# Optimization experiments

Hardware: AMD Instinct MI355X
Metric: run time of the kernel (lower is better)

The kernel has to match this reference:

```python
import jax, jax.numpy as jnp
import numpy as np

N, E, D = 50000, 800000, 64


def setup_inputs() -> dict:
    key = jax.random.key(0)
    ks = jax.random.split(key, 24)
    s = 1.0 / np.sqrt(D)
    inp = {
        'x': jax.random.normal(ks[0], (N, D), dtype=jnp.float32),
        'edge_index': jax.random.randint(ks[1], (2, E), 0, N, dtype=jnp.int32),
        'edge_attr_emb': jax.random.normal(ks[2], (E, D), dtype=jnp.float32),
    }
    names = ['Wq1', 'Wk1', 'Wv1', 'We1', 'Ws1', 'Wq2', 'Wk2', 'Wv2', 'We2', 'Ws2']
    for i, n in enumerate(names):
        inp[n] = jax.random.normal(ks[3 + i], (D, D), dtype=jnp.float32) * s
    for n in ['bq1', 'bk1', 'bv1', 'bs1', 'bq2', 'bk2', 'bv2', 'bs2']:
        inp[n] = jnp.zeros((D,), dtype=jnp.float32)
    return inp


def transformer_conv(x, src, dst, ea, Wq, bq, Wk, bk, Wv, bv, We, Ws, bs):
    # PyG TransformerConv, heads=1, concat=True, beta=False, root_weight=True
    q = x @ Wq + bq                      # [N, D]
    k = x @ Wk + bk                      # [N, D]
    v = x @ Wv + bv                      # [N, D]
    e = ea @ We                          # [E, D] (lin_edge has no bias)
    k_e = k[src] + e                     # gather source keys, modulate by edge
    logits = jnp.sum(q[dst] * k_e, axis=-1) / jnp.sqrt(jnp.asarray(D, x.dtype))  # [E]
    m = jax.ops.segment_max(logits, dst, num_segments=N)   # per-target max
    a = jnp.exp(logits - m[dst])
    denom = jax.ops.segment_sum(a, dst, num_segments=N)
    alpha = a / denom[dst]               # segment softmax over incoming edges
    msg = (v[src] + e) * alpha[:, None]  # [E, D]
    out = jax.ops.segment_sum(msg, dst, num_segments=N)    # scatter-add
    return out + x @ Ws + bs             # root/skip connection


def reference(x, edge_index, edge_attr_emb,
              Wq1, bq1, Wk1, bk1, Wv1, bv1, We1, Ws1, bs1,
              Wq2, bq2, Wk2, bk2, Wv2, bv2, We2, Ws2, bs2):
    src, dst = edge_index[0], edge_index[1]
    r = jax.nn.relu(x)
    r = transformer_conv(r, src, dst, edge_attr_emb, Wq1, bq1, Wk1, bk1, Wv1, bv1, We1, Ws1, bs1)
    r = jax.nn.relu(r)
    r = transformer_conv(r, src, dst, edge_attr_emb, Wq2, bq2, Wk2, bk2, Wv2, bv2, We2, Ws2, bs2)
    return x + r  # identity residual since l_in == l_out
```

## Files before the change

kernel.cpp:

```cpp
#include <hip/hip_runtime.h>
#include <math.h>

#define NN 50000
#define EE 800000
#define SCAN_B 196

__global__ __launch_bounds__(256) void k_hist(const int* __restrict__ ei,
                                              int* __restrict__ deg) {
    int i = blockIdx.x * 256 + threadIdx.x;
    if (i < EE) atomicAdd(&deg[ei[EE + i]], 1);
}

__global__ __launch_bounds__(256) void k_scanA(const int* __restrict__ deg,
                                               int* __restrict__ loc,
                                               int* __restrict__ bsum) {
    __shared__ int sh[256];
    int t = threadIdx.x, i = blockIdx.x * 256 + t;
    int v = (i < NN) ? deg[i] : 0;
    sh[t] = v;
    __syncthreads();
    for (int off = 1; off < 256; off <<= 1) {
        int u = (t >= off) ? sh[t - off] : 0;
        __syncthreads();
        sh[t] += u;
        __syncthreads();
    }
    if (i < NN) loc[i] = sh[t] - v;
    if (t == 255) bsum[blockIdx.x] = sh[255];
}

__global__ __launch_bounds__(256) void k_scanB(const int* __restrict__ bsum,
                                               int* __restrict__ boff) {
    __shared__ int sh[256];
    int t = threadIdx.x;
    int v = (t < SCAN_B) ? bsum[t] : 0;
    sh[t] = v;
    __syncthreads();
    for (int off = 1; off < 256; off <<= 1) {
        int u = (t >= off) ? sh[t - off] : 0;
        __syncthreads();
        sh[t] += u;
        __syncthreads();
    }
    if (t < SCAN_B) boff[t] = sh[t] - v;
}

__global__ __launch_bounds__(256) void k_scanC(const int* __restrict__ loc,
                                               const int* __restrict__ boff,
                                               int* __restrict__ rowptr,
                                               int* __restrict__ cursor) {
    int t = threadIdx.x, i = blockIdx.x * 256 + t;
    if (i < NN) {
        int r = loc[i] + boff[blockIdx.x];
        rowptr[i] = r;
        cursor[i] = r;
    }
    if (i == 0) rowptr[NN] = EE;
}

__global__ __launch_bounds__(256) void k_fill(const int* __restrict__ ei,
                                              int* __restrict__ cursor,
                                              int2* __restrict__ es) {
    int i = blockIdx.x * 256 + threadIdx.x;
    if (i < EE) {
        int d = ei[EE + i];
        int pos = atomicAdd(&cursor[d], 1);
        es[pos] = make_int2(ei[i], i);
    }
}

__global__ __launch_bounds__(64) void fuse_weights(
    const float* __restrict__ Wq, const float* __restrict__ We,
    const float* __restrict__ bq, float* __restrict__ Wqe,
    float* __restrict__ bqe) {
    int j = threadIdx.x;
    int t = blockIdx.x;
    if (t < 64) {
        float acc = 0.f;
        #pragma unroll
        for (int d = 0; d < 64; ++d) acc = fmaf(Wq[t * 64 + d], We[j * 64 + d], acc);
        Wqe[t * 64 + j] = acc;
    } else {
        float acc = 0.f;
        #pragma unroll
        for (int d = 0; d < 64; ++d) acc = fmaf(bq[d], We[j * 64 + d], acc);
        bqe[j] = acc;
    }
}

__global__ __launch_bounds__(256) void node_linear(
    const float* __restrict__ hin,
    const float* __restrict__ Wq, const float* __restrict__ Wk,
    const float* __restrict__ Wv, const float* __restrict__ Wsk,
    const float* __restrict__ Wqe,
    const float* __restrict__ bq, const float* __restrict__ bk,
    const float* __restrict__ bv, const float* __restrict__ bs,
    const float* __restrict__ bqe,
    float* __restrict__ q, float* __restrict__ k, float* __restrict__ v,
    float* __restrict__ skip, float* __restrict__ qe) {
    __shared__ float r[4][64];
    int wid = threadIdx.x >> 6, lane = threadIdx.x & 63;
    int n = blockIdx.x * 4 + wid;
    float xv = hin[n * 64 + lane];
    r[wid][lane] = xv > 0.f ? xv : 0.f;
    __syncthreads();
    float aq = 0.f, ak = 0.f, av = 0.f, as_ = 0.f, aqe = 0.f;
    #pragma unroll 8
    for (int j = 0; j < 64; ++j) {
        float rj = r[wid][j];
        aq  = fmaf(rj, Wq [j * 64 + lane], aq);
        ak  = fmaf(rj, Wk [j * 64 + lane], ak);
        av  = fmaf(rj, Wv [j * 64 + lane], av);
        as_ = fmaf(rj, Wsk[j * 64 + lane], as_);
        aqe = fmaf(rj, Wqe[j * 64 + lane], aqe);
    }
    int o = n * 64 + lane;
    q[o]    = aq  + bq[lane];
    k[o]    = ak  + bk[lane];
    v[o]    = av  + bv[lane];
    skip[o] = as_ + bs[lane];
    qe[o]   = aqe + bqe[lane];
}

__device__ __forceinline__ float dot4(float4 a, float4 b) {
    return fmaf(a.x, b.x, fmaf(a.y, b.y, fmaf(a.z, b.z, a.w * b.w)));
}
__device__ __forceinline__ float4 f4scale(float4 a, float s) {
    return make_float4(a.x * s, a.y * s, a.z * s, a.w * s);
}
__device__ __forceinline__ float4 f4fma(float s, float4 a, float4 acc) {
    return make_float4(fmaf(s, a.x, acc.x), fmaf(s, a.y, acc.y),
                       fmaf(s, a.z, acc.z), fmaf(s, a.w, acc.w));
}
__device__ __forceinline__ float4 f4shflxor_add(float4 a, int mask) {
    a.x += __shfl_xor(a.x, mask);
    a.y += __shfl_xor(a.y, mask);
    a.z += __shfl_xor(a.z, mask);
    a.w += __shfl_xor(a.w, mask);
    return a;
}

__global__ __launch_bounds__(256) void node_attn(
    const int* __restrict__ rowptr, const int2* __restrict__ es,
    const float* __restrict__ ea, const float* __restrict__ q,
    const float* __restrict__ k, const float* __restrict__ v,
    const float* __restrict__ qe, const float* __restrict__ skip,
    const float* __restrict__ We, const float* __restrict__ addx,
    float* __restrict__ out) {
    __shared__ float shA[4][64];
    __shared__ float shE[4][64];
    int wid = threadIdx.x >> 6, lane = threadIdx.x & 63;
    int g = lane >> 4, li = lane & 15;
    int n = blockIdx.x * 4 + wid;
    int beg = rowptr[n], end = rowptr[n + 1];

    const float4* q4  = (const float4*)q;
    const float4* qe4 = (const float4*)qe;
    const float4* k4  = (const float4*)k;
    const float4* v4  = (const float4*)v;
    const float4* ea4 = (const float4*)ea;

    float4 qd  = q4 [(size_t)n * 16 + li];
    float4 qed = qe4[(size_t)n * 16 + li];

    float m = -3.0e38f, den = 0.f;
    float4 av = make_float4(0, 0, 0, 0), ae = make_float4(0, 0, 0, 0);

    if (beg < end) {
        bool vldc; float4 kvc, vvc, evc;
        {
            int idx = beg + g; vldc = idx < end; int ci = vldc ? idx : beg;
            int2 se = es[ci];
            kvc = k4[(size_t)se.x * 16 + li];
            vvc = v4[(size_t)se.x * 16 + li];
            evc = ea4[(size_t)se.y * 16 + li];
        }
        for (int p = beg; p < end; p += 4) {
            bool vldn = false; float4 kvn, vvn, evn;
            if (p + 4 < end) {
                int idx = p + 4 + g; vldn = idx < end; int ci = vldn ? idx : beg;
                int2 se = es[ci];
                kvn = k4[(size_t)se.x * 16 + li];
                vvn = v4[(size_t)se.x * 16 + li];
                evn = ea4[(size_t)se.y * 16 + li];
            }
            float t = dot4(qd, kvc) + dot4(qed, evc);
            t += __shfl_xor(t, 1);
            t += __shfl_xor(t, 2);
            t += __shfl_xor(t, 4);
            t += __shfl_xor(t, 8);
            float lg = vldc ? t * 0.125f : -INFINITY;
            float mx = fmaxf(lg, __shfl_xor(lg, 16));
            mx = fmaxf(mx, __shfl_xor(mx, 32));
            if (mx > m) {
                float sc = __expf(m - mx);
                den *= sc; av = f4scale(av, sc); ae = f4scale(ae, sc);
                m = mx;
            }
            float a = __expf(lg - m);
            den += a;
            av = f4fma(a, vvc, av);
            ae = f4fma(a, evc, ae);
            vldc = vldn; kvc = kvn; vvc = vvn; evc = evn;
        }
    }
    av = f4shflxor_add(av, 16); av = f4shflxor_add(av, 32);
    ae = f4shflxor_add(ae, 16); ae = f4shflxor_add(ae, 32);
    den += __shfl_xor(den, 16); den += __shfl_xor(den, 32);
    if (lane < 16) {
        *(float4*)&shA[wid][lane * 4] = av;
        *(float4*)&shE[wid][lane * 4] = ae;
    }
    __syncthreads();
    float r = 0.f;
    #pragma unroll 8
    for (int j = 0; j < 64; ++j) r = fmaf(shE[wid][j], We[j * 64 + lane], r);
    size_t no = (size_t)n * 64 + lane;
    float o = (den > 0.f) ? (shA[wid][lane] + r) / den : 0.f;
    o += skip[no];
    if (addx) o += addx[no];
    out[no] = o;
}

extern "C" void kernel_launch(void* const* d_in, const int* in_sizes, int n_in,
                              void* d_out, int out_size, void* d_ws, size_t ws_size,
                              hipStream_t stream) {
    const float* x  = (const float*)d_in[0];
    const int*   ei = (const int*)d_in[1];
    const float* ea = (const float*)d_in[2];
    const float* W[10];
    for (int i = 0; i < 10; ++i) W[i] = (const float*)d_in[3 + i];
    const float* B[8];
    for (int i = 0; i < 8; ++i) B[i] = (const float*)d_in[13 + i];

    const size_t ND = (size_t)NN * 64;
    float* ws   = (float*)d_ws;
    float* q    = ws;
    float* k    = ws + 1 * ND;
    float* v    = ws + 2 * ND;
    float* skip = ws + 3 * ND;
    float* qe   = ws + 4 * ND;
    float* h    = ws + 5 * ND;
    int* deg    = (int*)(ws + 6 * ND);
    int* loc    = deg + NN;
    int* bsum   = loc + NN;
    int* boff   = bsum + 256;
    int* rowptr = boff + 256;
    int* cursor = rowptr + NN + 1;
    int2* es    = (int2*)(cursor + NN + 1);
    float* Wqe  = (float*)(es + EE);
    float* bqe  = Wqe + 4096;

    (void)hipMemsetAsync(deg, 0, NN * sizeof(int), stream);
    k_hist <<<(EE + 255) / 256, 256, 0, stream>>>(ei, deg);
    k_scanA<<<SCAN_B, 256, 0, stream>>>(deg, loc, bsum);
    k_scanB<<<1, 256, 0, stream>>>(bsum, boff);
    k_scanC<<<SCAN_B, 256, 0, stream>>>(loc, boff, rowptr, cursor);
    k_fill <<<(EE + 255) / 256, 256, 0, stream>>>(ei, cursor, es);

    for (int l = 0; l < 2; ++l) {
        const float* Wq = W[l * 5 + 0], *Wk = W[l * 5 + 1], *Wv = W[l * 5 + 2];
        const float* We = W[l * 5 + 3], *Wsk = W[l * 5 + 4];
        const float* bq = B[l * 4 + 0], *bk = B[l * 4 + 1];
        const float* bv = B[l * 4 + 2], *bs = B[l * 4 + 3];

        fuse_weights<<<65, 64, 0, stream>>>(Wq, We, bq, Wqe, bqe);
        node_linear<<<NN / 4, 256, 0, stream>>>(
            l ? h : x, Wq, Wk, Wv, Wsk, Wqe, bq, bk, bv, bs, bqe,
            q, k, v, skip, qe);
        node_attn<<<NN / 4, 256, 0, stream>>>(
            rowptr, es, ea, q, k, v, qe, skip, We,
            l ? x : nullptr, l ? (float*)d_out : h);
    }
}
```

Baseline: 898.1 us.

## Tile node_linear over 128 nodes with register-resident weight columns per wave

Rewrites the node projection kernel so each block stages 128 ReLU'd node rows in shared memory. Each of five waves keeps one weight matrix's column (64 floats) in registers and sweeps all staged nodes two at a time. This removes the repeated global/L2 weight reads per node in the old per-node layout, in exchange for far fewer blocks (391), higher register pressure, and shared-memory broadcast reads.

```diff
diff --git a/kernel.cpp b/kernel.cpp
--- a/kernel.cpp
+++ b/kernel.cpp
@@ -4,6 +4,8 @@
 #define NN 50000
 #define EE 800000
 #define SCAN_B 196
+#define NPB 128
+#define NLT 320
 
 __global__ __launch_bounds__(256) void k_hist(const int* __restrict__ ei,
                                               int* __restrict__ deg) {
@@ -88,7 +90,7 @@
     }
 }
 
-__global__ __launch_bounds__(256) void node_linear(
+__global__ __launch_bounds__(NLT) void node_linear(
     const float* __restrict__ hin,
     const float* __restrict__ Wq, const float* __restrict__ Wk,
     const float* __restrict__ Wv, const float* __restrict__ Wsk,
@@ -98,28 +100,68 @@
     const float* __restrict__ bqe,
     float* __restrict__ q, float* __restrict__ k, float* __restrict__ v,
     float* __restrict__ skip, float* __restrict__ qe) {
-    __shared__ float r[4][64];
-    int wid = threadIdx.x >> 6, lane = threadIdx.x & 63;
-    int n = blockIdx.x * 4 + wid;
-    float xv = hin[n * 64 + lane];
-    r[wid][lane] = xv > 0.f ? xv : 0.f;
+    __shared__ float rt[NPB * 64];
+    int tid = threadIdx.x;
+    int n0 = blockIdx.x * NPB;
+    int cnt = min(NPB, NN - n0);
+
+    const float4* hin4 = (const float4*)hin + (size_t)n0 * 16;
+    float4* rt4 = (float4*)rt;
+    int tot4 = cnt * 16;
+    for (int i = tid; i < tot4; i += NLT) {
+        float4 xv = hin4[i];
+        rt4[i] = make_float4(fmaxf(xv.x, 0.f), fmaxf(xv.y, 0.f),
+                             fmaxf(xv.z, 0.f), fmaxf(xv.w, 0.f));
+    }
     __syncthreads();
-    float aq = 0.f, ak = 0.f, av = 0.f, as_ = 0.f, aqe = 0.f;
-    #pragma unroll 8
-    for (int j = 0; j < 64; ++j) {
-        float rj = r[wid][j];
-        aq  = fmaf(rj, Wq [j * 64 + lane], aq);
-        ak  = fmaf(rj, Wk [j * 64 + lane], ak);
-        av  = fmaf(rj, Wv [j * 64 + lane], av);
-        as_ = fmaf(rj, Wsk[j * 64 + lane], as_);
-        aqe = fmaf(rj, Wqe[j * 64 + lane], aqe);
-    }
-    int o = n * 64 + lane;
-    q[o]    = aq  + bq[lane];
-    k[o]    = ak  + bk[lane];
-    v[o]    = av  + bv[lane];
-    skip[o] = as_ + bs[lane];
-    qe[o]   = aqe + bqe[lane];
+
+    int wid = tid >> 6, lane = tid & 63;
+    const float* Wsel = wid == 0 ? Wq : wid == 1 ? Wk : wid == 2 ? Wv
+                      : wid == 3 ? Wsk : Wqe;
+    const float* bsel = wid == 0 ? bq : wid == 1 ? bk : wid == 2 ? bv
+                      : wid == 3 ? bs : bqe;
+    float*       osel = wid == 0 ? q  : wid == 1 ? k  : wid == 2 ? v
+                      : wid == 3 ? skip : qe;
+    float bias = bsel[lane];
+
+    float4 w[16];
+    #pragma unroll
+    for (int jj = 0; jj < 16; ++jj) {
+        w[jj].x = Wsel[(jj * 4 + 0) * 64 + lane];
+        w[jj].y = Wsel[(jj * 4 + 1) * 64 + lane];
+        w[jj].z = Wsel[(jj * 4 + 2) * 64 + lane];
+        w[jj].w = Wsel[(jj * 4 + 3) * 64 + lane];
+    }
+
+    for (int b = 0; b < cnt; b += 2) {
+        bool has1 = (b + 1) < cnt;
+        const float4* r0 = (const float4*)&rt[b * 64];
+        const float4* r1 = (const float4*)&rt[(has1 ? b + 1 : b) * 64];
+        float a0 = bias, a0b = 0.f, a1 = bias, a1b = 0.f;
+        #pragma unroll
+        for (int jj = 0; jj < 16; jj += 2) {
+            float4 rb0 = r0[jj],     rb1 = r1[jj];
+            float4 rc0 = r0[jj + 1], rc1 = r1[jj + 1];
+            a0  = fmaf(rb0.x, w[jj].x, a0);
+            a0  = fmaf(rb0.y, w[jj].y, a0);
+            a0  = fmaf(rb0.z, w[jj].z, a0);
+            a0  = fmaf(rb0.w, w[jj].w, a0);
+            a0b = fmaf(rc0.x, w[jj + 1].x, a0b);
+            a0b = fmaf(rc0.y, w[jj + 1].y, a0b);
+            a0b = fmaf(rc0.z, w[jj + 1].z, a0b);
+            a0b = fmaf(rc0.w, w[jj + 1].w, a0b);
+            a1  = fmaf(rb1.x, w[jj].x, a1);
+            a1  = fmaf(rb1.y, w[jj].y, a1);
+            a1  = fmaf(rb1.z, w[jj].z, a1);
+            a1  = fmaf(rb1.w, w[jj].w, a1);
+            a1b = fmaf(rc1.x, w[jj + 1].x, a1b);
+            a1b = fmaf(rc1.y, w[jj + 1].y, a1b);
+            a1b = fmaf(rc1.z, w[jj + 1].z, a1b);
+            a1b = fmaf(rc1.w, w[jj + 1].w, a1b);
+        }
+        osel[(size_t)(n0 + b) * 64 + lane] = a0 + a0b;
+        if (has1) osel[(size_t)(n0 + b + 1) * 64 + lane] = a1 + a1b;
+    }
 }
 
 __device__ __forceinline__ float dot4(float4 a, float4 b) {
@@ -265,7 +307,7 @@
         const float* bv = B[l * 4 + 2], *bs = B[l * 4 + 3];
 
         fuse_weights<<<65, 64, 0, stream>>>(Wq, We, bq, Wqe, bqe);
-        node_linear<<<NN / 4, 256, 0, stream>>>(
+        node_linear<<<(NN + NPB - 1) / NPB, NLT, 0, stream>>>(
             l ? h : x, Wq, Wk, Wv, Wsk, Wqe, bq, bk, bv, bs, bqe,
             q, k, v, skip, qe);
         node_attn<<<NN / 4, 256, 0, stream>>>(
```

Measured after the change: 1.194 ms. 32.9% more time.
